# Optimization experiments

Measured on AMD Instinct MI355X. Metric: run time of the kernel, lower is better.

Reference implementation:

```python
import jax, jax.numpy as jnp
import numpy as np

N = 100000   # nodes
E = 1600000  # edges
D = 64       # hidden_channels
H = 2 * D    # MLP expansion
L = 4        # num_layers
G = 64       # graphs in batch
OUT = 1      # out_channels
LN_EPS = 1e-5


def layer_norm(h, gamma, beta):
    mu = jnp.mean(h, axis=-1, keepdims=True)
    var = jnp.var(h, axis=-1, keepdims=True)
    return (h - mu) * jax.lax.rsqrt(var + LN_EPS) * gamma + beta


def setup_inputs() -> dict:
    key = jax.random.key(0)
    ks = jax.random.split(key, 16)
    s = 0.05
    x = jax.random.normal(ks[0], (N, D), jnp.float32)
    edge_index = jax.random.randint(ks[1], (2, E), 0, N)
    batch = jnp.sort(jax.random.randint(ks[2], (N,), 0, G))
    # lin_in
    W_in = jax.random.normal(ks[3], (D, D), jnp.float32) * s
    b_in = jnp.zeros((D,), jnp.float32)
    # per-layer GINConv params (stacked over L layers)
    eps = jnp.zeros((L,), jnp.float32)
    W1 = jax.random.normal(ks[4], (L, D, H), jnp.float32) * s
    b1 = jnp.zeros((L, H), jnp.float32)
    gamma = jnp.ones((L, H), jnp.float32)
    beta = jnp.zeros((L, H), jnp.float32)
    W2 = jax.random.normal(ks[5], (L, H, D), jnp.float32) * s
    b2 = jnp.zeros((L, D), jnp.float32)
    # lin_out MLP
    Wo1 = jax.random.normal(ks[6], (D, H), jnp.float32) * s
    bo1 = jnp.zeros((H,), jnp.float32)
    Wo2 = jax.random.normal(ks[7], (H, OUT), jnp.float32) * s
    bo2 = jnp.zeros((OUT,), jnp.float32)
    return {
        "x": x, "W_in": W_in, "b_in": b_in, "eps": eps,
        "W1": W1, "b1": b1, "gamma": gamma, "beta": beta,
        "W2": W2, "b2": b2, "Wo1": Wo1, "bo1": bo1,
        "Wo2": Wo2, "bo2": bo2,
        "edge_index": edge_index, "batch": batch,
    }


def gin_conv(h, edge_index, eps_l, W1_l, b1_l, gamma_l, beta_l, W2_l, b2_l):
    src = edge_index[0]  # x_j
    dst = edge_index[1]  # aggregation target i
    # message = relu(x_j); aggr = scatter-add into dst
    agg = jax.ops.segment_sum(jax.nn.relu(h[src]), dst, num_segments=N)
    z = (1.0 + eps_l) * h + agg
    z = z @ W1_l + b1_l
    z = jax.nn.relu(layer_norm(z, gamma_l, beta_l))
    return z @ W2_l + b2_l


def reference(x, W_in, b_in, eps, W1, b1, gamma, beta, W2, b2,
              Wo1, bo1, Wo2, bo2, edge_index, batch):
    h = x @ W_in + b_in  # [N, D]
    for i in range(L):
        h = h + gin_conv(h, edge_index, eps[i], W1[i], b1[i],
                         gamma[i], beta[i], W2[i], b2[i])
        # dropout p=0.0 -> identity
    pooled = jax.ops.segment_sum(h, batch, num_segments=G)  # [G, D]
    out = jax.nn.relu(pooled @ Wo1 + bo1) @ Wo2 + bo2        # [G, OUT]
    return out.reshape(-1)
```

## Files before the change

kernel.cpp:

```cpp
#include <hip/hip_runtime.h>
#include <hip/hip_bf16.h>

#define NN 100000
#define NE 1600000
#define DD 64
#define HH 128
#define NLAYERS 4
#define NGRAPH 64
#define NBUCKET 782
#define NCHUNK 391
#define NTOT (NBUCKET * NCHUNK)

typedef __attribute__((ext_vector_type(8))) short bf16x8;
typedef __attribute__((ext_vector_type(4))) float f32x4;

__device__ inline unsigned short bf16bits(float v) {
  return __bfloat16_as_ushort(__float2bfloat16(v));
}


__global__ void k_hist(const int* __restrict__ dst, int* __restrict__ hist) {
  __shared__ int lh[NBUCKET];
  int t = threadIdx.x;
  int blk = blockIdx.x;
  for (int i = t; i < NBUCKET; i += 256) lh[i] = 0;
  __syncthreads();
  int cb = blk * 4096;
  int end = min(cb + 4096, NE);
  for (int i = cb + t; i < end; i += 256)
    atomicAdd(&lh[dst[i] >> 7], 1);
  __syncthreads();
  for (int i = t; i < NBUCKET; i += 256)
    hist[i * NCHUNK + blk] = lh[i];
}

__global__ void k_scan1(const int* __restrict__ in, int* __restrict__ out,
                        int* __restrict__ bsum, int n) {
  __shared__ int s[256];
  int t = threadIdx.x;
  int i = blockIdx.x * 256 + t;
  int v = (i < n) ? in[i] : 0;
  s[t] = v;
  __syncthreads();
  for (int off = 1; off < 256; off <<= 1) {
    int x = (t >= off) ? s[t - off] : 0;
    __syncthreads();
    s[t] += x;
    __syncthreads();
  }
  if (i < n) out[i] = s[t] - v;
  if (t == 255) bsum[blockIdx.x] = s[255];
}

__global__ void k_scan2b(int* bsum, int nb) {
  __shared__ int s[256];
  int t = threadIdx.x;
  int base = t * 5;
  int v[5];
  int sum = 0;
#pragma unroll
  for (int j = 0; j < 5; j++) {
    int i = base + j;
    v[j] = (i < nb) ? bsum[i] : 0;
    sum += v[j];
  }
  s[t] = sum;
  __syncthreads();
  for (int off = 1; off < 256; off <<= 1) {
    int x = (t >= off) ? s[t - off] : 0;
    __syncthreads();
    s[t] += x;
    __syncthreads();
  }
  int ex = s[t] - sum;
#pragma unroll
  for (int j = 0; j < 5; j++) {
    int i = base + j;
    if (i < nb) { int vv = v[j]; bsum[i] = ex; ex += vv; }
  }
}

__global__ void k_scan3b(int* __restrict__ hist, const int* __restrict__ bsum,
                         int* __restrict__ bbase, int n) {
  int i = blockIdx.x * 256 + threadIdx.x;
  if (i < n) {
    int v = hist[i] + bsum[i >> 8];
    hist[i] = v;
    if (i % NCHUNK == 0) bbase[i / NCHUNK] = v;
  }
}

__global__ void k_scatter(const int* __restrict__ src, const int* __restrict__ dst,
                          const int* __restrict__ hist, unsigned int* __restrict__ tmp) {
  __shared__ int lcur[NBUCKET];
  int t = threadIdx.x;
  int blk = blockIdx.x;
  for (int i = t; i < NBUCKET; i += 256) lcur[i] = hist[i * NCHUNK + blk];
  __syncthreads();
  int cb = blk * 4096;
  int end = min(cb + 4096, NE);
  for (int i = cb + t; i < end; i += 256) {
    int d = dst[i];
    int pos = atomicAdd(&lcur[d >> 7], 1);
    tmp[pos] = ((unsigned int)(d & 127) << 20) | (unsigned int)src[i];
  }
}

__global__ void k_fillB2(const unsigned int* __restrict__ tmp,
                         const int* __restrict__ bbase,
                         int* __restrict__ csr, int* __restrict__ offs,
                         int* __restrict__ cnt) {
  __shared__ int lcnt[128], lex[128], lcur[128];
  int b = blockIdx.x;
  int t = threadIdx.x;
  int base = bbase[b];
  int end = (b == NBUCKET - 1) ? NE : bbase[b + 1];
  if (t < 128) lcnt[t] = 0;
  __syncthreads();
  for (int i = base + t; i < end; i += 256)
    atomicAdd(&lcnt[tmp[i] >> 20], 1);
  __syncthreads();
  int v = (t < 128) ? lcnt[t] : 0;
  if (t < 128) lex[t] = v;
  __syncthreads();
  for (int off = 1; off < 128; off <<= 1) {
    int x = (t >= off && t < 128) ? lex[t - off] : 0;
    __syncthreads();
    if (t < 128) lex[t] += x;
    __syncthreads();
  }
  if (t < 128) {
    int ex = lex[t] - v;
    lcur[t] = ex;
    int node = (b << 7) + t;
    if (node < NN) { offs[node] = base + ex; cnt[node] = v; }
  }
  __syncthreads();
  for (int i = base + t; i < end; i += 256) {
    unsigned int u = tmp[i];
    int dl = u >> 20;
    int pos = atomicAdd(&lcur[dl], 1);
    csr[base + pos] = u & 0xFFFFF;
  }
}

__global__ void k_prep(const float* __restrict__ W1, const float* __restrict__ W2,
                       const float* __restrict__ W_in,
                       unsigned short* __restrict__ W1t, unsigned short* __restrict__ W2t,
                       unsigned short* __restrict__ Wint) {
  int bidx = blockIdx.x;
  int t = threadIdx.x;
  if (bidx == 2 * NLAYERS) {
    for (int i = t; i < 4096; i += 256) {
      int c = i >> 6, k = i & 63;
      Wint[i] = bf16bits(W_in[k * 64 + c]);
    }
    return;
  }
  int l = bidx >> 1;
  int m = bidx & 1;
  if (m == 0) {
    const float* src = W1 + (size_t)l * 8192;
    unsigned short* dstp = W1t + (size_t)l * 8192;
    for (int i = t; i < 8192; i += 256) {
      int c = i >> 6, k = i & 63;
      dstp[i] = bf16bits(src[k * 128 + c]);
    }
  } else {
    const float* src = W2 + (size_t)l * 8192;
    unsigned short* dstp = W2t + (size_t)l * 8192;
    for (int i = t; i < 8192; i += 256) {
      int c = i >> 7, k = i & 127;
      dstp[i] = bf16bits(src[k * 64 + c]);
    }
  }
}

__global__ __launch_bounds__(256) void k_lin(
    const float* __restrict__ x, const unsigned short* __restrict__ Wint,
    const float* __restrict__ binp, float* __restrict__ h,
    unsigned short* __restrict__ rh) {
  __shared__ __align__(16) unsigned short sW[4096];
  __shared__ float sb[64];
  int t = threadIdx.x;
  {
    const uint4* wg = (const uint4*)Wint;
    uint4* sWu = (uint4*)sW;
    for (int g = t; g < 512; g += 256) {
      int c = g >> 3, s = g & 7;
      sWu[c * 8 + (s ^ (c & 7))] = wg[g];
    }
    if (t < 64) sb[t] = binp[t];
  }
  int l = t & 63, w = t >> 6, lm = l & 15, lk = l >> 4;
  int rowl = w * 16 + lm;
  int grow = blockIdx.x * 64 + rowl;
  int growc = min(grow, NN - 1);
  bf16x8 a[2];
#pragma unroll
  for (int kb = 0; kb < 2; kb++) {
    const float* xp = &x[(size_t)growc * 64 + kb * 32 + lk * 8];
    float4 x0 = *(const float4*)xp;
    float4 x1 = *(const float4*)(xp + 4);
    a[kb][0] = (short)bf16bits(x0.x); a[kb][1] = (short)bf16bits(x0.y);
    a[kb][2] = (short)bf16bits(x0.z); a[kb][3] = (short)bf16bits(x0.w);
    a[kb][4] = (short)bf16bits(x1.x); a[kb][5] = (short)bf16bits(x1.y);
    a[kb][6] = (short)bf16bits(x1.z); a[kb][7] = (short)bf16bits(x1.w);
  }
  __syncthreads();
  f32x4 acc[4];
#pragma unroll
  for (int n = 0; n < 4; n++) {
    float bc = sb[n * 16 + lm];
    acc[n] = (f32x4){bc, bc, bc, bc};
  }
  const bf16x8* sWf = (const bf16x8*)sW;
#pragma unroll
  for (int n = 0; n < 4; n++) {
    int c = n * 16 + lm;
    bf16x8 b0 = sWf[c * 8 + ((0 * 4 + lk) ^ (c & 7))];
    bf16x8 b1 = sWf[c * 8 + ((1 * 4 + lk) ^ (c & 7))];
    acc[n] = __builtin_amdgcn_mfma_f32_16x16x32_bf16(a[0], b0, acc[n], 0, 0, 0);
    acc[n] = __builtin_amdgcn_mfma_f32_16x16x32_bf16(a[1], b1, acc[n], 0, 0, 0);
  }
#pragma unroll
  for (int r = 0; r < 4; r++) {
    int grow2 = blockIdx.x * 64 + w * 16 + lk * 4 + r;
    if (grow2 < NN) {
#pragma unroll
      for (int n = 0; n < 4; n++) {
        int c = n * 16 + lm;
        size_t idx = (size_t)grow2 * 64 + c;
        float o = acc[n][r];
        h[idx] = o;
        rh[idx] = bf16bits(fmaxf(o, 0.f));
      }
    }
  }
}

__global__ __launch_bounds__(256) void k_fused(
    float* __restrict__ h, const unsigned short* __restrict__ rhin,
    unsigned short* __restrict__ rhout,
    const int* __restrict__ csr, const int* __restrict__ offs,
    const int* __restrict__ cnt,
    const unsigned short* __restrict__ W1t, const float* __restrict__ b1l,
    const float* __restrict__ gl, const float* __restrict__ btl,
    const unsigned short* __restrict__ W2t, const float* __restrict__ b2l,
    const float* __restrict__ epsl) {
  __shared__ __align__(16) unsigned short sW[8192];
  __shared__ __align__(16) unsigned short sRr[8192];
  __shared__ float sb1[128], sg[128], sbt[128], sb2[64];

  int t = threadIdx.x;
  int nbase = blockIdx.x * 64;
  int l = t & 63;
  int w = t >> 6;
  int lm = l & 15;
  int lk = l >> 4;

  {
    const uint4* w1g = (const uint4*)W1t;
    uint4* sWu = (uint4*)sW;
    for (int g = t; g < 1024; g += 256) {
      int c = g >> 3, s = g & 7;
      sWu[c * 8 + (s ^ (c & 7))] = w1g[g];
    }
    if (t < 128) { sb1[t] = b1l[t]; sg[t] = gl[t]; sbt[t] = btl[t]; }
    if (t < 64) sb2[t] = b2l[t];
  }
  float epsv = 1.0f + *epsl;

  int rowl = w * 16 + lm;
  int grow = nbase + rowl;
  int growc = min(grow, NN - 1);
  int start = offs[growc];
  int deg = (grow < NN) ? cnt[growc] : 0;

  const float* hp = &h[(size_t)growc * 64 + lk * 8];
  float4 hv0 = *(const float4*)hp;
  float4 hv1 = *(const float4*)(hp + 4);
  float4 hv2 = *(const float4*)(hp + 32);
  float4 hv3 = *(const float4*)(hp + 36);

  float accA[8] = {0.f, 0.f, 0.f, 0.f, 0.f, 0.f, 0.f, 0.f};
  float accB[8] = {0.f, 0.f, 0.f, 0.f, 0.f, 0.f, 0.f, 0.f};
  for (int j0 = 0; j0 < deg; j0 += 8) {
    int idxA = csr[start + j0 + lk];
    int idxB = csr[start + j0 + 4 + lk];
    int c8 = deg - j0;
    int ss[8];
#pragma unroll
    for (int jj = 0; jj < 4; jj++) ss[jj] = __shfl(idxA, lm + jj * 16);
#pragma unroll
    for (int jj = 0; jj < 4; jj++) ss[4 + jj] = __shfl(idxB, lm + jj * 16);
    uint4 va[8], vb[8];
#pragma unroll
    for (int jj = 0; jj < 8; jj++) {
      const unsigned short* rp = rhin + (size_t)ss[jj] * 64 + lk * 8;
      va[jj] = *(const uint4*)rp;
      vb[jj] = *(const uint4*)(rp + 32);
    }
#pragma unroll
    for (int jj = 0; jj < 8; jj++) {
      if (jj < c8) {
        uint4 vA = va[jj], vB = vb[jj];
        accA[0] += __uint_as_float(vA.x << 16);
        accA[1] += __uint_as_float(vA.x & 0xFFFF0000u);
        accA[2] += __uint_as_float(vA.y << 16);
        accA[3] += __uint_as_float(vA.y & 0xFFFF0000u);
        accA[4] += __uint_as_float(vA.z << 16);
        accA[5] += __uint_as_float(vA.z & 0xFFFF0000u);
        accA[6] += __uint_as_float(vA.w << 16);
        accA[7] += __uint_as_float(vA.w & 0xFFFF0000u);
        accB[0] += __uint_as_float(vB.x << 16);
        accB[1] += __uint_as_float(vB.x & 0xFFFF0000u);
        accB[2] += __uint_as_float(vB.y << 16);
        accB[3] += __uint_as_float(vB.y & 0xFFFF0000u);
        accB[4] += __uint_as_float(vB.z << 16);
        accB[5] += __uint_as_float(vB.z & 0xFFFF0000u);
        accB[6] += __uint_as_float(vB.w << 16);
        accB[7] += __uint_as_float(vB.w & 0xFFFF0000u);
      }
    }
  }

  bf16x8 a1[2];
  {
    const float* h0p = &hv0.x;
    const float* h1p = &hv2.x;
#pragma unroll
    for (int j = 0; j < 4; j++) {
      a1[0][j] = (short)bf16bits(epsv * h0p[j] + accA[j]);
      a1[0][4 + j] = (short)bf16bits(epsv * (&hv1.x)[j] + accA[4 + j]);
      a1[1][j] = (short)bf16bits(epsv * h1p[j] + accB[j]);
      a1[1][4 + j] = (short)bf16bits(epsv * (&hv3.x)[j] + accB[4 + j]);
    }
  }
  __syncthreads();

  f32x4 acc1[8];
#pragma unroll
  for (int n = 0; n < 8; n++) {
    float bc = sb1[n * 16 + lm];
    acc1[n] = (f32x4){bc, bc, bc, bc};
  }
  {
    const bf16x8* sW1f = (const bf16x8*)sW;
#pragma unroll
    for (int n = 0; n < 8; n++) {
      int c = n * 16 + lm;
      bf16x8 b0 = sW1f[c * 8 + ((0 * 4 + lk) ^ (c & 7))];
      bf16x8 b1f = sW1f[c * 8 + ((1 * 4 + lk) ^ (c & 7))];
      acc1[n] = __builtin_amdgcn_mfma_f32_16x16x32_bf16(a1[0], b0, acc1[n], 0, 0, 0);
      acc1[n] = __builtin_amdgcn_mfma_f32_16x16x32_bf16(a1[1], b1f, acc1[n], 0, 0, 0);
    }
  }

  float psr[4], pqr[4];
#pragma unroll
  for (int r = 0; r < 4; r++) {
    float s = 0.f, q = 0.f;
#pragma unroll
    for (int n = 0; n < 8; n++) { float v = acc1[n][r]; s += v; q += v * v; }
    psr[r] = s; pqr[r] = q;
  }
#pragma unroll
  for (int m = 1; m <= 8; m <<= 1) {
#pragma unroll
    for (int r = 0; r < 4; r++) {
      psr[r] += __shfl_xor(psr[r], m);
      pqr[r] += __shfl_xor(pqr[r], m);
    }
  }
#pragma unroll
  for (int r = 0; r < 4; r++) {
    float mu = psr[r] * (1.0f / 128.0f);
    float var = pqr[r] * (1.0f / 128.0f) - mu * mu;
    float rs = rsqrtf(var + 1e-5f);
    int rowr = w * 16 + lk * 4 + r;
#pragma unroll
    for (int n = 0; n < 8; n++) {
      int c = n * 16 + lm;
      float v = (acc1[n][r] - mu) * rs * sg[c] + sbt[c];
      v = fmaxf(v, 0.f);
      int slot = (c >> 3) ^ (rowr & 7);
      sRr[rowr * 128 + slot * 8 + (c & 7)] = bf16bits(v);
    }
  }
  __syncthreads();

  {
    const uint4* w2g = (const uint4*)W2t;
    uint4* sWu = (uint4*)sW;
    for (int g = t; g < 1024; g += 256) {
      int c = g >> 4, s = g & 15;
      sWu[c * 16 + (s ^ (c & 15))] = w2g[g];
    }
  }
  __syncthreads();

  f32x4 acc2[4];
#pragma unroll
  for (int n2 = 0; n2 < 4; n2++) {
    float bc = sb2[n2 * 16 + lm];
    acc2[n2] = (f32x4){bc, bc, bc, bc};
  }
  {
    const bf16x8* sRf = (const bf16x8*)sRr;
    const bf16x8* sW2f = (const bf16x8*)sW;
    bf16x8 a2[4];
#pragma unroll
    for (int kb = 0; kb < 4; kb++)
      a2[kb] = sRf[rowl * 16 + ((kb * 4 + lk) ^ (rowl & 7))];
#pragma unroll
    for (int n2 = 0; n2 < 4; n2++) {
      int c = n2 * 16 + lm;
#pragma unroll
      for (int kb = 0; kb < 4; kb++) {
        bf16x8 bfr = sW2f[c * 16 + ((kb * 4 + lk) ^ (c & 15))];
        acc2[n2] = __builtin_amdgcn_mfma_f32_16x16x32_bf16(a2[kb], bfr, acc2[n2], 0, 0, 0);
      }
    }
  }

#pragma unroll
  for (int r = 0; r < 4; r++) {
    int grow2 = nbase + w * 16 + lk * 4 + r;
    if (grow2 < NN) {
#pragma unroll
      for (int n2 = 0; n2 < 4; n2++) {
        int c = n2 * 16 + lm;
        size_t idx = (size_t)grow2 * 64 + c;
        float o = h[idx] + acc2[n2][r];
        h[idx] = o;
        rhout[idx] = bf16bits(fmaxf(o, 0.f));
      }
    }
  }
}

__global__ void k_pool(const float* __restrict__ h, const int* __restrict__ batch,
                       float* __restrict__ pooled, int n) {
  int t = threadIdx.x;
  int d = t & 63;
  int w = t >> 6;
  int n0 = blockIdx.x * 256 + w * 64;
  float acc = 0.f;
  int prev = -1;
  for (int i = 0; i < 64; i++) {
    int nn = n0 + i;
    if (nn >= n) break;
    int g = batch[nn];
    if (g != prev) {
      if (prev >= 0) atomicAdd(&pooled[prev * 64 + d], acc);
      prev = g;
      acc = 0.f;
    }
    acc += h[(size_t)nn * 64 + d];
  }
  if (prev >= 0) atomicAdd(&pooled[prev * 64 + d], acc);
}

__global__ __launch_bounds__(128) void k_out(
    const float* __restrict__ pooled, const float* __restrict__ Wo1,
    const float* __restrict__ bo1, const float* __restrict__ Wo2,
    const float* __restrict__ bo2, float* __restrict__ out) {
  __shared__ __align__(16) float sP[64];
  __shared__ float sPart[2];
  int g = blockIdx.x;
  int c = threadIdx.x;
  if (c < 64) sP[c] = pooled[g * 64 + c];
  __syncthreads();
  float t1 = bo1[c];
#pragma unroll 8
  for (int k = 0; k < 64; k++) t1 += sP[k] * Wo1[k * 128 + c];
  float v = fmaxf(t1, 0.f) * Wo2[c];
#pragma unroll
  for (int m = 1; m <= 32; m <<= 1) v += __shfl_xor(v, m);
  if ((c & 63) == 0) sPart[c >> 6] = v;
  __syncthreads();
  if (c == 0) out[g] = sPart[0] + sPart[1] + bo2[0];
}


static inline char* align_up(char* p, size_t a) {
  return (char*)(((uintptr_t)p + a - 1) & ~(uintptr_t)(a - 1));
}

extern "C" void kernel_launch(void* const* d_in, const int* in_sizes, int n_in,
                              void* d_out, int out_size, void* d_ws, size_t ws_size,
                              hipStream_t stream) {
  const float* x    = (const float*)d_in[0];
  const float* W_in = (const float*)d_in[1];
  const float* b_in = (const float*)d_in[2];
  const float* eps  = (const float*)d_in[3];
  const float* W1   = (const float*)d_in[4];
  const float* b1   = (const float*)d_in[5];
  const float* gam  = (const float*)d_in[6];
  const float* bet  = (const float*)d_in[7];
  const float* W2   = (const float*)d_in[8];
  const float* b2   = (const float*)d_in[9];
  const float* Wo1  = (const float*)d_in[10];
  const float* bo1  = (const float*)d_in[11];
  const float* Wo2  = (const float*)d_in[12];
  const float* bo2  = (const float*)d_in[13];
  const int* ei     = (const int*)d_in[14];
  const int* batch  = (const int*)d_in[15];
  float* out = (float*)d_out;

  const int* e_src = ei;
  const int* e_dst = ei + NE;

  char* p = (char*)d_ws;
  float* h = (float*)p;                     p += (size_t)NN * 64 * 4;
  unsigned short* rh0 = (unsigned short*)p; p += (size_t)NN * 64 * 2;
  unsigned short* rh1 = (unsigned short*)p;
  unsigned int* tmp = (unsigned int*)p;
                                            p += (size_t)NN * 64 * 2;
  int* csr = (int*)p;
  int* hist = (int*)p;
                                            p += (size_t)NE * 4;
  int* offs = (int*)p;                      p += (size_t)NN * 4;
  int* cnt = (int*)p;                       p += (size_t)NN * 4;
  int* bsumH = (int*)p;                     p += 1280 * 4;
  int* bbase = (int*)p;                     p += (NBUCKET + 1) * 4;
  p = align_up(p, 256);
  float* pooled = (float*)p;                p += (size_t)NGRAPH * 64 * 4;
  p = align_up(p, 256);
  unsigned short* W1t = (unsigned short*)p; p += (size_t)NLAYERS * 8192 * 2;
  unsigned short* W2t = (unsigned short*)p; p += (size_t)NLAYERS * 8192 * 2;
  unsigned short* Wint = (unsigned short*)p; p += 4096 * 2;

  const int SCAN_BLOCKS_H = (NTOT + 255) / 256;
  const int NODE_BLOCKS = (NN + 63) / 64;

  hipMemsetAsync(pooled, 0, (size_t)NGRAPH * 64 * 4, stream);

  k_hist<<<NCHUNK, 256, 0, stream>>>(e_dst, hist);
  k_scan1<<<SCAN_BLOCKS_H, 256, 0, stream>>>(hist, hist, bsumH, NTOT);
  k_scan2b<<<1, 256, 0, stream>>>(bsumH, SCAN_BLOCKS_H);
  k_scan3b<<<SCAN_BLOCKS_H, 256, 0, stream>>>(hist, bsumH, bbase, NTOT);
  k_scatter<<<NCHUNK, 256, 0, stream>>>(e_src, e_dst, hist, tmp);
  k_fillB2<<<NBUCKET, 256, 0, stream>>>(tmp, bbase, csr, offs, cnt);

  k_prep<<<NLAYERS * 2 + 1, 256, 0, stream>>>(W1, W2, W_in, W1t, W2t, Wint);
  k_lin<<<NODE_BLOCKS, 256, 0, stream>>>(x, Wint, b_in, h, rh0);

  for (int l = 0; l < NLAYERS; l++) {
    unsigned short* rin  = (l & 1) ? rh1 : rh0;
    unsigned short* rout = (l & 1) ? rh0 : rh1;
    k_fused<<<NODE_BLOCKS, 256, 0, stream>>>(h, rin, rout, csr, offs, cnt,
        W1t + (size_t)l * 8192, b1 + (size_t)l * 128,
        gam + (size_t)l * 128, bet + (size_t)l * 128,
        W2t + (size_t)l * 8192, b2 + (size_t)l * 64,
        eps + l);
  }

  k_pool<<<(NN + 255) / 256, 256, 0, stream>>>(h, batch, pooled, NN);
  k_out<<<NGRAPH, 128, 0, stream>>>(pooled, Wo1, bo1, Wo2, bo2, out);
}
```

Measured before the change: 347.5 us.

## Store node features only in bf16, apply relu at gather time

Drops the fp32 residual buffer `h` and the separate relu'd bf16 copy. A single pre-relu bf16 feature buffer is now ping-ponged across layers, and relu is applied on the fly while aggregating neighbours. This removes the fp32 read and write of h per layer and one bf16 write, which should cut memory traffic in the fused layer, lin and pool kernels. Out-of-range gather lanes now load a valid neighbour row instead of stale indices. The cost is that the residual stream is kept in bf16, which loses precision across the four layers.

Measured after the change: 339.6 us. 2.3% less time.

```diff
diff --git a/kernel.cpp b/kernel.cpp
--- a/kernel.cpp
+++ b/kernel.cpp
@@ -17,6 +17,9 @@
 __device__ inline unsigned short bf16bits(float v) {
   return __bfloat16_as_ushort(__float2bfloat16(v));
 }
+__device__ inline float lo16(unsigned int u) { return __uint_as_float(u << 16); }
+__device__ inline float hi16(unsigned int u) { return __uint_as_float(u & 0xFFFF0000u); }
+__device__ inline float b2f(unsigned short u) { return __uint_as_float(((unsigned int)u) << 16); }
 
 
 __global__ void k_hist(const int* __restrict__ dst, int* __restrict__ hist) {
@@ -178,8 +181,7 @@
 
 __global__ __launch_bounds__(256) void k_lin(
     const float* __restrict__ x, const unsigned short* __restrict__ Wint,
-    const float* __restrict__ binp, float* __restrict__ h,
-    unsigned short* __restrict__ rh) {
+    const float* __restrict__ binp, unsigned short* __restrict__ hout) {
   __shared__ __align__(16) unsigned short sW[4096];
   __shared__ float sb[64];
   int t = threadIdx.x;
@@ -230,18 +232,14 @@
 #pragma unroll
       for (int n = 0; n < 4; n++) {
         int c = n * 16 + lm;
-        size_t idx = (size_t)grow2 * 64 + c;
-        float o = acc[n][r];
-        h[idx] = o;
-        rh[idx] = bf16bits(fmaxf(o, 0.f));
+        hout[(size_t)grow2 * 64 + c] = bf16bits(acc[n][r]);
       }
     }
   }
 }
 
 __global__ __launch_bounds__(256) void k_fused(
-    float* __restrict__ h, const unsigned short* __restrict__ rhin,
-    unsigned short* __restrict__ rhout,
+    const unsigned short* __restrict__ hin, unsigned short* __restrict__ hout,
     const int* __restrict__ csr, const int* __restrict__ offs,
     const int* __restrict__ cnt,
     const unsigned short* __restrict__ W1t, const float* __restrict__ b1l,
@@ -277,11 +275,9 @@
   int start = offs[growc];
   int deg = (grow < NN) ? cnt[growc] : 0;
 
-  const float* hp = &h[(size_t)growc * 64 + lk * 8];
-  float4 hv0 = *(const float4*)hp;
-  float4 hv1 = *(const float4*)(hp + 4);
-  float4 hv2 = *(const float4*)(hp + 32);
-  float4 hv3 = *(const float4*)(hp + 36);
+  const unsigned short* hp = hin + (size_t)growc * 64 + lk * 8;
+  uint4 hva = *(const uint4*)hp;
+  uint4 hvb = *(const uint4*)(hp + 32);
 
   float accA[8] = {0.f, 0.f, 0.f, 0.f, 0.f, 0.f, 0.f, 0.f};
   float accB[8] = {0.f, 0.f, 0.f, 0.f, 0.f, 0.f, 0.f, 0.f};
@@ -297,7 +293,8 @@
     uint4 va[8], vb[8];
 #pragma unroll
     for (int jj = 0; jj < 8; jj++) {
-      const unsigned short* rp = rhin + (size_t)ss[jj] * 64 + lk * 8;
+      int s = (jj < c8) ? ss[jj] : ss[0];
+      const unsigned short* rp = hin + (size_t)s * 64 + lk * 8;
       va[jj] = *(const uint4*)rp;
       vb[jj] = *(const uint4*)(rp + 32);
     }
@@ -305,37 +302,37 @@
     for (int jj = 0; jj < 8; jj++) {
       if (jj < c8) {
         uint4 vA = va[jj], vB = vb[jj];
-        accA[0] += __uint_as_float(vA.x << 16);
-        accA[1] += __uint_as_float(vA.x & 0xFFFF0000u);
-        accA[2] += __uint_as_float(vA.y << 16);
-        accA[3] += __uint_as_float(vA.y & 0xFFFF0000u);
-        accA[4] += __uint_as_float(vA.z << 16);
-        accA[5] += __uint_as_float(vA.z & 0xFFFF0000u);
-        accA[6] += __uint_as_float(vA.w << 16);
-        accA[7] += __uint_as_float(vA.w & 0xFFFF0000u);
-        accB[0] += __uint_as_float(vB.x << 16);
-        accB[1] += __uint_as_float(vB.x & 0xFFFF0000u);
-        accB[2] += __uint_as_float(vB.y << 16);
-        accB[3] += __uint_as_float(vB.y & 0xFFFF0000u);
-        accB[4] += __uint_as_float(vB.z << 16);
-        accB[5] += __uint_as_float(vB.z & 0xFFFF0000u);
-        accB[6] += __uint_as_float(vB.w << 16);
-        accB[7] += __uint_as_float(vB.w & 0xFFFF0000u);
+        accA[0] += fmaxf(lo16(vA.x), 0.f);
+        accA[1] += fmaxf(hi16(vA.x), 0.f);
+        accA[2] += fmaxf(lo16(vA.y), 0.f);
+        accA[3] += fmaxf(hi16(vA.y), 0.f);
+        accA[4] += fmaxf(lo16(vA.z), 0.f);
+        accA[5] += fmaxf(hi16(vA.z), 0.f);
+        accA[6] += fmaxf(lo16(vA.w), 0.f);
+        accA[7] += fmaxf(hi16(vA.w), 0.f);
+        accB[0] += fmaxf(lo16(vB.x), 0.f);
+        accB[1] += fmaxf(hi16(vB.x), 0.f);
+        accB[2] += fmaxf(lo16(vB.y), 0.f);
+        accB[3] += fmaxf(hi16(vB.y), 0.f);
+        accB[4] += fmaxf(lo16(vB.z), 0.f);
+        accB[5] += fmaxf(hi16(vB.z), 0.f);
+        accB[6] += fmaxf(lo16(vB.w), 0.f);
+        accB[7] += fmaxf(hi16(vB.w), 0.f);
       }
     }
   }
 
   bf16x8 a1[2];
   {
-    const float* h0p = &hv0.x;
-    const float* h1p = &hv2.x;
-#pragma unroll
-    for (int j = 0; j < 4; j++) {
-      a1[0][j] = (short)bf16bits(epsv * h0p[j] + accA[j]);
-      a1[0][4 + j] = (short)bf16bits(epsv * (&hv1.x)[j] + accA[4 + j]);
-      a1[1][j] = (short)bf16bits(epsv * h1p[j] + accB[j]);
-      a1[1][4 + j] = (short)bf16bits(epsv * (&hv3.x)[j] + accB[4 + j]);
-    }
+    float hz[8];
+    hz[0] = lo16(hva.x); hz[1] = hi16(hva.x); hz[2] = lo16(hva.y); hz[3] = hi16(hva.y);
+    hz[4] = lo16(hva.z); hz[5] = hi16(hva.z); hz[6] = lo16(hva.w); hz[7] = hi16(hva.w);
+#pragma unroll
+    for (int j = 0; j < 8; j++) a1[0][j] = (short)bf16bits(epsv * hz[j] + accA[j]);
+    hz[0] = lo16(hvb.x); hz[1] = hi16(hvb.x); hz[2] = lo16(hvb.y); hz[3] = hi16(hvb.y);
+    hz[4] = lo16(hvb.z); hz[5] = hi16(hvb.z); hz[6] = lo16(hvb.w); hz[7] = hi16(hvb.w);
+#pragma unroll
+    for (int j = 0; j < 8; j++) a1[1][j] = (short)bf16bits(epsv * hz[j] + accB[j]);
   }
   __syncthreads();
 
@@ -432,15 +429,15 @@
       for (int n2 = 0; n2 < 4; n2++) {
         int c = n2 * 16 + lm;
         size_t idx = (size_t)grow2 * 64 + c;
-        float o = h[idx] + acc2[n2][r];
-        h[idx] = o;
-        rhout[idx] = bf16bits(fmaxf(o, 0.f));
+        float o = b2f(hin[idx]) + acc2[n2][r];
+        hout[idx] = bf16bits(o);
       }
     }
   }
 }
 
-__global__ void k_pool(const float* __restrict__ h, const int* __restrict__ batch,
+__global__ void k_pool(const unsigned short* __restrict__ h,
+                       const int* __restrict__ batch,
                        float* __restrict__ pooled, int n) {
   int t = threadIdx.x;
   int d = t & 63;
@@ -457,7 +454,7 @@
       prev = g;
       acc = 0.f;
     }
-    acc += h[(size_t)nn * 64 + d];
+    acc += b2f(h[(size_t)nn * 64 + d]);
   }
   if (prev >= 0) atomicAdd(&pooled[prev * 64 + d], acc);
 }
@@ -513,9 +510,8 @@
   const int* e_dst = ei + NE;
 
   char* p = (char*)d_ws;
-  float* h = (float*)p;                     p += (size_t)NN * 64 * 4;
-  unsigned short* rh0 = (unsigned short*)p; p += (size_t)NN * 64 * 2;
-  unsigned short* rh1 = (unsigned short*)p;
+  unsigned short* hA = (unsigned short*)p;  p += (size_t)NN * 64 * 2;
+  unsigned short* hB = (unsigned short*)p;
   unsigned int* tmp = (unsigned int*)p;
                                             p += (size_t)NN * 64 * 2;
   int* csr = (int*)p;
@@ -545,18 +541,18 @@
   k_fillB2<<<NBUCKET, 256, 0, stream>>>(tmp, bbase, csr, offs, cnt);
 
   k_prep<<<NLAYERS * 2 + 1, 256, 0, stream>>>(W1, W2, W_in, W1t, W2t, Wint);
-  k_lin<<<NODE_BLOCKS, 256, 0, stream>>>(x, Wint, b_in, h, rh0);
+  k_lin<<<NODE_BLOCKS, 256, 0, stream>>>(x, Wint, b_in, hA);
 
   for (int l = 0; l < NLAYERS; l++) {
-    unsigned short* rin  = (l & 1) ? rh1 : rh0;
-    unsigned short* rout = (l & 1) ? rh0 : rh1;
-    k_fused<<<NODE_BLOCKS, 256, 0, stream>>>(h, rin, rout, csr, offs, cnt,
+    const unsigned short* hin = (l & 1) ? hB : hA;
+    unsigned short* ho = (l & 1) ? hA : hB;
+    k_fused<<<NODE_BLOCKS, 256, 0, stream>>>(hin, ho, csr, offs, cnt,
         W1t + (size_t)l * 8192, b1 + (size_t)l * 128,
         gam + (size_t)l * 128, bet + (size_t)l * 128,
         W2t + (size_t)l * 8192, b2 + (size_t)l * 64,
         eps + l);
   }
 
-  k_pool<<<(NN + 255) / 256, 256, 0, stream>>>(h, batch, pooled, NN);
+  k_pool<<<(NN + 255) / 256, 256, 0, stream>>>(hA, batch, pooled, NN);
   k_out<<<NGRAPH, 128, 0, stream>>>(pooled, Wo1, bo1, Wo2, bo2, out);
 }
```
